# Performance work log

Measured on AMD Instinct MI355X. Metric: run time of the kernel, lower is better.

Reference implementation:

```python
import jax, jax.numpy as jnp
import numpy as np
from jax import lax

# dims: B batch, L seq len, D channels, N SSM state size
BATCH, L, D, N = 8, 2048, 256, 64
MIN_DELTA = 1e-6
EPS = 1e-6


def setup_inputs() -> dict:
    key = jax.random.key(0)
    k0, k1, k2, k3, k4 = jax.random.split(key, 5)
    x = jax.random.normal(k0, (BATCH, L, D), dtype=jnp.float32)
    # log_A chosen so A = softplus(log_A) is small -> discrete_A^L stays finite in fp32
    log_A = -jax.random.normal(k1, (N, N), dtype=jnp.float32) - 3.0
    Bp = jax.random.normal(k2, (D, N), dtype=jnp.float32) * 0.02
    Cp = jax.random.normal(k3, (D, N), dtype=jnp.float32) * 0.02
    log_delta = jnp.full((D,), -8.0, dtype=jnp.float32)  # dt ~ 3.4e-4 (stability)
    skip_D = jnp.ones((D,), dtype=jnp.float32)
    W_out = jax.random.normal(k4, (D, D), dtype=jnp.float32) * (1.0 / np.sqrt(D))
    b_out = jnp.zeros((D,), dtype=jnp.float32)
    return dict(x=x, log_A=log_A, Bp=Bp, Cp=Cp, log_delta=log_delta,
                skip_D=skip_D, W_out=W_out, b_out=b_out)


def reference(x, log_A, Bp, Cp, log_delta, skip_D, W_out, b_out):
    Bsz, Lx, Dx = x.shape
    # --- discretize ---
    A = jax.nn.softplus(log_A)                                  # [N,N]
    dt = jax.nn.softplus(log_delta) + MIN_DELTA                 # [D]
    dA = jax.vmap(jax.scipy.linalg.expm)(A[None] * dt[:, None, None])  # [D,N,N]
    I = jnp.eye(A.shape[0], dtype=A.dtype)
    X = jnp.linalg.solve(A + EPS * I, Bp.T)                     # [N,D] = A^{-1} B^T
    dB = jnp.einsum('dnm,dm->dn', dA - I, X.T)                  # [D,N]
    # --- kernel k[d,l] = C_d . (dA_d)^l dB_d, via sequential recurrence (same math
    # as the explicit A-power loop, carrying the vector instead of the matrix) ---
    def step(v, _):
        return jnp.einsum('dnm,dm->dn', dA, v), jnp.sum(Cp * v, axis=-1)
    _, ks = lax.scan(step, dB, None, length=Lx)                 # ks: [L,D]
    k = ks.T                                                    # [D,L]
    # --- grouped causal conv1d: y[b,d,t] = sum_tau k[d,tau] x[b,d,t-tau] ---
    w = jnp.flip(k, -1)[:, None, :]                             # [D,1,L]
    y = lax.conv_general_dilated(
        jnp.transpose(x, (0, 2, 1)), w, (1,), [(Lx - 1, 0)],
        dimension_numbers=('NCH', 'OIH', 'NCH'), feature_group_count=Dx)
    y = jnp.transpose(y, (0, 2, 1))                             # [B,L,D]
    return (y + x * skip_D) @ W_out.T + b_out
```

## Files before the change

kernel.cpp:

```cpp
#include <hip/hip_runtime.h>

#define Bz 8
#define Lz 2048
#define Dz 256
#define Nz 64
#define SP 68
#define SA 65
#define SAK 72
#define SKB 136
#define SE 68
#define KE 4
#define KP 7

typedef __attribute__((ext_vector_type(8))) short bf16x8;
typedef __attribute__((ext_vector_type(4))) float f32x4;

__device__ __forceinline__ float softplusf(float x) {
  return (x > 20.f) ? x : log1pf(expf(x));
}

__device__ __forceinline__ unsigned short f2bf(float f) {
  unsigned int u = __float_as_uint(f);
  u += 0x7fffu + ((u >> 16) & 1u);
  return (unsigned short)(u >> 16);
}

__device__ __forceinline__ void pmm_acc(const float* __restrict__ LA,
                                        const float* __restrict__ LB,
                                        float* acc, int n, int q) {
  float arow[64];
#pragma unroll
  for (int mm = 0; mm < 16; ++mm) {
    const float4 a4 = *(const float4*)(LA + n * SP + mm * 4);
    arow[4 * mm + 0] = a4.x; arow[4 * mm + 1] = a4.y;
    arow[4 * mm + 2] = a4.z; arow[4 * mm + 3] = a4.w;
  }
#pragma unroll
  for (int i = 0; i < 16; ++i) acc[i] = 0.f;
#pragma unroll 8
  for (int m = 0; m < 64; ++m) {
    const float4 b0 = *(const float4*)(LB + m * SP + q * 16 + 0);
    const float4 b1 = *(const float4*)(LB + m * SP + q * 16 + 4);
    const float4 b2 = *(const float4*)(LB + m * SP + q * 16 + 8);
    const float4 b3 = *(const float4*)(LB + m * SP + q * 16 + 12);
    const float a = arow[m];
    acc[0]  = fmaf(a, b0.x, acc[0]);  acc[1]  = fmaf(a, b0.y, acc[1]);
    acc[2]  = fmaf(a, b0.z, acc[2]);  acc[3]  = fmaf(a, b0.w, acc[3]);
    acc[4]  = fmaf(a, b1.x, acc[4]);  acc[5]  = fmaf(a, b1.y, acc[5]);
    acc[6]  = fmaf(a, b1.z, acc[6]);  acc[7]  = fmaf(a, b1.w, acc[7]);
    acc[8]  = fmaf(a, b2.x, acc[8]);  acc[9]  = fmaf(a, b2.y, acc[9]);
    acc[10] = fmaf(a, b2.z, acc[10]); acc[11] = fmaf(a, b2.w, acc[11]);
    acc[12] = fmaf(a, b3.x, acc[12]); acc[13] = fmaf(a, b3.y, acc[13]);
    acc[14] = fmaf(a, b3.z, acc[14]); acc[15] = fmaf(a, b3.w, acc[15]);
  }
}

__global__ __launch_bounds__(256) void s4_xt(const float* __restrict__ x,
                                             float* __restrict__ xT,
                                             const float* __restrict__ log_A,
                                             float* __restrict__ Apow) {
  if (blockIdx.x == 0 && blockIdx.y == 0) {
    const int i = blockIdx.z * 512 + threadIdx.x;
    Apow[i] = softplusf(log_A[i]);
    Apow[i + 256] = softplusf(log_A[i + 256]);
  }
  __shared__ float tile[64][69];
  const int t0 = blockIdx.x * 64, d0 = blockIdx.y * 64, b = blockIdx.z;
  const int rr = threadIdx.x >> 4;
  const int c4 = (threadIdx.x & 15) * 4;
#pragma unroll
  for (int p = 0; p < 4; ++p) {
    const int row = p * 16 + rr;
    const float4 v = *(const float4*)(x + ((size_t)b * Lz + t0 + row) * Dz + d0 + c4);
    tile[row][c4 + 0] = v.x; tile[row][c4 + 1] = v.y;
    tile[row][c4 + 2] = v.z; tile[row][c4 + 3] = v.w;
  }
  __syncthreads();
#pragma unroll
  for (int p = 0; p < 4; ++p) {
    const int dd = p * 16 + rr;
    float4 o;
    o.x = tile[c4 + 0][dd]; o.y = tile[c4 + 1][dd];
    o.z = tile[c4 + 2][dd]; o.w = tile[c4 + 3][dd];
    *(float4*)(xT + ((size_t)(d0 + dd) * Bz + b) * Lz + t0 + c4) = o;
  }
}

__global__ __launch_bounds__(256, 1) void s4_buildpow(
    float* __restrict__ Apow, const float* __restrict__ Bp,
    const float* __restrict__ Cp, const float* __restrict__ log_delta,
    float* __restrict__ Gk, float* __restrict__ Qk,
    float* __restrict__ kloc, float* __restrict__ dts) {
  __shared__ float As[Nz * SA];
  __shared__ float Pst[KP + 1][Nz];
  __shared__ float Qst[KE + 1][Nz];
  __shared__ float Pv[Nz], Qv[Nz], dBs[Nz];
  __shared__ float prA[4][Nz + 8], prB[4][Nz + 8];
  __shared__ float zp[KE + 1][17], zs[KE + 1];
  __shared__ alignas(16) float PA[Nz * SP];
  __shared__ alignas(16) float PB[Nz * SP];
  const int tid = threadIdx.x;
  const int d = blockIdx.x;
  const int n = tid & 63, qq = tid >> 6;

  if (d >= Dz) {
    const int role = d - Dz;
#pragma unroll
    for (int i = 0; i < 4; ++i) {
      const int e = (tid + 256 * i) * 4;
      const int r = e >> 6, c = e & 63;
      const float4 v = *(const float4*)(Apow + e);
      *(float4*)&PA[r * SP + c] = v;
      *(float4*)&PB[r * SP + c] = v;
    }
    __syncthreads();
    float acc[16];
    pmm_acc(PA, PB, acc, n, qq);
    if (role == 0) {
      float* O = Apow + (size_t)1 * 4096;
#pragma unroll
      for (int v = 0; v < 4; ++v) {
        float4 o;
        o.x = acc[4 * v]; o.y = acc[4 * v + 1];
        o.z = acc[4 * v + 2]; o.w = acc[4 * v + 3];
        *(float4*)(O + n * 64 + qq * 16 + 4 * v) = o;
      }
      return;
    }
    __syncthreads();
#pragma unroll
    for (int i = 0; i < 16; ++i) {
      PB[n * SP + qq * 16 + i] = acc[i];
      if (role == 2) PA[n * SP + qq * 16 + i] = acc[i];
    }
    __syncthreads();
    pmm_acc(PA, PB, acc, n, qq);
    float* O = Apow + (size_t)(role + 1) * 4096;
#pragma unroll
    for (int v = 0; v < 4; ++v) {
      float4 o;
      o.x = acc[4 * v]; o.y = acc[4 * v + 1];
      o.z = acc[4 * v + 2]; o.w = acc[4 * v + 3];
      *(float4*)(O + n * 64 + qq * 16 + 4 * v) = o;
    }
    return;
  }

  const float dt = softplusf(log_delta[d]) + 1e-6f;
#pragma unroll
  for (int i = 0; i < 4; ++i) {
    const int e = (tid + 256 * i) * 4;
    const int r = e >> 6, c = e & 63;
    const float4 v = *(const float4*)(Apow + e);
    As[r * SA + c] = v.x; As[r * SA + c + 1] = v.y;
    As[r * SA + c + 2] = v.z; As[r * SA + c + 3] = v.w;
  }
  if (tid < 64) {
    const float bv = Bp[d * Nz + tid], cv = Cp[d * Nz + tid];
    Pv[tid] = bv; Pst[0][tid] = bv;
    Qv[tid] = cv; Qst[0][tid] = cv;
  }
  __syncthreads();
#pragma unroll 1
  for (int k = 1; k <= KP; ++k) {
    float pp = 0.f, pq = 0.f;
#pragma unroll
    for (int mm = 0; mm < 16; ++mm) {
      const int m = qq * 16 + mm;
      pp += As[n * SA + m] * Pv[m];
      pq += As[m * SA + n] * Qv[m];
    }
    prA[qq][n] = pp; prB[qq][n] = pq;
    __syncthreads();
    if (tid < 64) {
      const float np = prA[0][tid] + prA[1][tid] + prA[2][tid] + prA[3][tid];
      Pv[tid] = np; Pst[k][tid] = np;
      if (k <= KE) {
        const float nq = prB[0][tid] + prB[1][tid] + prB[2][tid] + prB[3][tid];
        Qv[tid] = nq; Qst[k][tid] = nq;
      }
    }
    __syncthreads();
  }
  const float dtc0 = dt;
  const float dtc1 = dt * dt * 0.5f;
  const float dtc2 = dtc1 * dt * (1.f / 3.f);
  const float dtc3 = dtc2 * dt * 0.25f;
  if (tid < 64) {
    dBs[tid] = dtc0 * Pst[0][tid] + dtc1 * Pst[1][tid] +
               dtc2 * Pst[2][tid] + dtc3 * Pst[3][tid];
#pragma unroll
    for (int k = 0; k <= KE; ++k) {
      Gk[(size_t)d * ((KE + 1) * 64) + k * 64 + tid] =
          dtc0 * Pst[k][tid] + dtc1 * Pst[k + 1][tid] +
          dtc2 * Pst[k + 2][tid] + dtc3 * Pst[k + 3][tid];
      Qk[(size_t)d * ((KE + 1) * 64) + k * 64 + tid] = Qst[k][tid];
    }
  }
  __syncthreads();
  if (tid < (KE + 1) * 16) {
    const int k = tid >> 4, seg = tid & 15;
    float s = 0.f;
#pragma unroll
    for (int i = 0; i < 4; ++i) s += Qst[k][seg * 4 + i] * dBs[seg * 4 + i];
    zp[k][seg] = s;
  }
  __syncthreads();
  if (tid <= KE) {
    float s = 0.f;
#pragma unroll
    for (int seg = 0; seg < 16; ++seg) s += zp[tid][seg];
    zs[tid] = s;
  }
  __syncthreads();
  if (tid < 64) {
    const float rdt = (float)tid * dt;
    float c = 1.f, acc = zs[0];
#pragma unroll
    for (int k = 1; k <= KE; ++k) { c *= rdt / (float)k; acc += c * zs[k]; }
    kloc[d * 64 + tid] = acc;
  }
  if (tid == 0) dts[d] = dt;
}

__global__ __launch_bounds__(512, 2) void s4_scan7(
    const float* __restrict__ xT, const float* __restrict__ Apow,
    const float* __restrict__ Gk, const float* __restrict__ dts,
    float* __restrict__ S) {
  __shared__ alignas(16) float Es[Nz * SE];
  __shared__ alignas(16) float Us[Nz * SE];
  __shared__ float Gs[(KE + 1) * Nz];
  __shared__ float CTs[KE + 1][66];
  __shared__ alignas(16) float Sw[Bz][SE];
  __shared__ alignas(16) float Xw[Bz][SE];
  const int d = blockIdx.x;
  const int tid = threadIdx.x;
  const int w = tid >> 6;
  const int n = tid & 63;
  const float dt = dts[d];
  if (tid < 65) {
    const float rdt = (float)tid * dt;
    float c = 1.f;
    CTs[0][tid] = 1.f;
#pragma unroll
    for (int k = 1; k <= KE; ++k) { c *= rdt / (float)k; CTs[k][tid] = c; }
  }
  for (int idx = tid; idx < (KE + 1) * 64; idx += 512)
    Gs[idx] = Gk[(size_t)d * ((KE + 1) * 64) + idx];
  {
    float ea[8];
#pragma unroll
    for (int i = 0; i < 8; ++i) ea[i] = 0.f;
    const float dt64 = 64.f * dt;
    float ce = 1.f;
#pragma unroll
    for (int k = 1; k <= KE; ++k) {
      ce *= dt64 / (float)k;
      const float* Ak = Apow + (size_t)(k - 1) * 4096;
#pragma unroll
      for (int i = 0; i < 8; ++i)
        ea[i] = fmaf(ce, Ak[tid + 512 * i], ea[i]);
    }
#pragma unroll
    for (int i = 0; i < 8; ++i) {
      const int e = tid + 512 * i;
      const int r = e >> 6, c = e & 63;
      Es[r * SE + c] = ea[i] + ((r == c) ? 1.f : 0.f);
    }
  }
  __syncthreads();
  {
    const int r = tid >> 3, j0 = (tid & 7) * 8;
    float g0 = Gs[0 * 64 + r], g1 = Gs[1 * 64 + r], g2 = Gs[2 * 64 + r];
    float g3 = Gs[3 * 64 + r], g4 = Gs[4 * 64 + r];
#pragma unroll
    for (int jj = 0; jj < 8; ++jj) {
      const int j = j0 + jj;
      float u = g0 * CTs[0][63 - j];
      u = fmaf(g1, CTs[1][63 - j], u);
      u = fmaf(g2, CTs[2][63 - j], u);
      u = fmaf(g3, CTs[3][63 - j], u);
      u = fmaf(g4, CTs[4][63 - j], u);
      Us[r * SE + j] = u;
    }
  }
  __syncthreads();
  float Erow[64], Urow[64];
#pragma unroll
  for (int mb = 0; mb < 16; ++mb) {
    const float4 e4 = *(const float4*)&Es[n * SE + 4 * mb];
    Erow[4 * mb + 0] = e4.x; Erow[4 * mb + 1] = e4.y;
    Erow[4 * mb + 2] = e4.z; Erow[4 * mb + 3] = e4.w;
    const float4 u4 = *(const float4*)&Us[n * SE + 4 * mb];
    Urow[4 * mb + 0] = u4.x; Urow[4 * mb + 1] = u4.y;
    Urow[4 * mb + 2] = u4.z; Urow[4 * mb + 3] = u4.w;
  }
  const float* xw = xT + ((size_t)d * Bz + w) * (size_t)Lz;
  float* Sd = S + (size_t)d * (32 * 8 * 64) + w * 64 + n;
  float s = 0.f;
  float xcur = xw[n];
  float xnxt = xw[64 + n];
#pragma unroll 1
  for (int c = 0; c < 32; ++c) {
    Sw[w][n] = s;
    Xw[w][n] = xcur;
    Sd[(size_t)c * 512] = s;
    const int cl = (c + 2 < 32) ? (c + 2) : 31;
    const float xnew = xw[cl * 64 + n];
    float a0 = 0.f, a1 = 0.f, a2 = 0.f, a3 = 0.f;
#pragma unroll
    for (int mb = 0; mb < 16; ++mb) {
      const float4 sb = *(const float4*)&Sw[w][4 * mb];
      a0 = fmaf(Erow[4 * mb + 0], sb.x, a0);
      a1 = fmaf(Erow[4 * mb + 1], sb.y, a1);
      a2 = fmaf(Erow[4 * mb + 2], sb.z, a2);
      a3 = fmaf(Erow[4 * mb + 3], sb.w, a3);
    }
#pragma unroll
    for (int jb = 0; jb < 16; ++jb) {
      const float4 xb = *(const float4*)&Xw[w][4 * jb];
      a0 = fmaf(Urow[4 * jb + 0], xb.x, a0);
      a1 = fmaf(Urow[4 * jb + 1], xb.y, a1);
      a2 = fmaf(Urow[4 * jb + 2], xb.z, a2);
      a3 = fmaf(Urow[4 * jb + 3], xb.w, a3);
    }
    s = (a0 + a1) + (a2 + a3);
    xcur = xnxt; xnxt = xnew;
  }
}

__global__ __launch_bounds__(256, 4) void s4_out7(
    const float* __restrict__ xT, const float* __restrict__ S,
    const float* __restrict__ Qk, const float* __restrict__ kloc,
    const float* __restrict__ dts, const float* __restrict__ skip_D,
    unsigned short* __restrict__ yb) {
  __shared__ alignas(16) unsigned short Msb[64 * SKB];
  __shared__ alignas(16) unsigned short Zsb[64 * SKB];
  __shared__ float Qs[(KE + 1) * Nz];
  __shared__ float CT[KE + 1][66];
  __shared__ unsigned short kxb[64];
  const int d = blockIdx.x;
  const int ch = blockIdx.y;
  const int tid = threadIdx.x;
  const int wave = tid >> 6, lane = tid & 63;
  const int quad = lane >> 4, lq = lane & 15;
  const float dt = dts[d];
  if (tid < 65) {
    const float rdt = (float)tid * dt;
    float c = 1.f;
    CT[0][tid] = 1.f;
#pragma unroll
    for (int k = 1; k <= KE; ++k) { c *= rdt / (float)k; CT[k][tid] = c; }
  }
  for (int idx = tid; idx < (KE + 1) * 64; idx += 256)
    Qs[idx] = Qk[(size_t)d * ((KE + 1) * 64) + idx];
  if (tid < 64)
    kxb[tid] = f2bf(kloc[d * 64 + tid] + ((tid == 0) ? skip_D[d] : 0.f));

  const float* xd = xT + (size_t)d * Bz * Lz;
  const float* Sd = S + (size_t)d * (32 * 8 * 64);
#pragma unroll
  for (int p = 0; p < 8; ++p) {
    const int u = tid + 256 * p;
    const int col = u >> 5;
    const int sub = u & 31;
    const int k0 = sub * 4;
    const int bb = col & 7, ccl = col >> 3;
    const int cc = ch * 8 + ccl;
    const float* src = (k0 < 64)
        ? (Sd + cc * 512 + bb * 64 + k0)
        : (xd + (size_t)bb * Lz + cc * 64 + (k0 - 64));
    const float4 v = *(const float4*)src;
    ushort4 o;
    o.x = f2bf(v.x); o.y = f2bf(v.y); o.z = f2bf(v.z); o.w = f2bf(v.w);
    *(ushort4*)&Zsb[col * SKB + k0] = o;
  }
  __syncthreads();

#pragma unroll
  for (int i = 0; i < 16; ++i) {
    const int e = tid + 256 * i;
    const int r = e >> 6, m = e & 63;
    float w = 0.f;
#pragma unroll
    for (int k = 0; k <= KE; ++k) w = fmaf(CT[k][r + 1], Qs[k * 64 + m], w);
    Msb[r * SKB + m] = f2bf(w);
  }
#pragma unroll
  for (int i = 0; i < 16; ++i) {
    const int e = tid + 256 * i;
    const int r = e >> 6, j = e & 63;
    Msb[r * SKB + 64 + j] = (j <= r) ? kxb[r - j] : (unsigned short)0;
  }
  __syncthreads();

  f32x4 acc[4];
#pragma unroll
  for (int ni = 0; ni < 4; ++ni)
#pragma unroll
    for (int i = 0; i < 4; ++i) acc[ni][i] = 0.f;
#pragma unroll
  for (int ks = 0; ks < 4; ++ks) {
    const bf16x8 af =
        *(const bf16x8*)&Msb[(wave * 16 + lq) * SKB + ks * 32 + quad * 8];
#pragma unroll
    for (int ni = 0; ni < 4; ++ni) {
      const bf16x8 bfr =
          *(const bf16x8*)&Zsb[(ni * 16 + lq) * SKB + ks * 32 + quad * 8];
      acc[ni] = __builtin_amdgcn_mfma_f32_16x16x32_bf16(af, bfr, acc[ni], 0, 0, 0);
    }
  }
#pragma unroll
  for (int ni = 0; ni < 4; ++ni) {
    const int col = ni * 16 + lq;
    const int bb = col & 7, ccl = col >> 3;
    const int cc = ch * 8 + ccl;
    ushort4 o;
    o.x = f2bf(acc[ni][0]); o.y = f2bf(acc[ni][1]);
    o.z = f2bf(acc[ni][2]); o.w = f2bf(acc[ni][3]);
    *(ushort4*)(yb + ((size_t)d * Bz + bb) * Lz + cc * 64 + wave * 16 + quad * 4) = o;
  }
}

__global__ __launch_bounds__(256, 2) void s4_gemm5(
    const unsigned short* __restrict__ yb, const float* __restrict__ Wo,
    const float* __restrict__ bo, float* __restrict__ out) {
  __shared__ alignas(16) unsigned short LA[128 * SAK];
  __shared__ alignas(16) unsigned short LB[64 * SAK];
  const int tid = threadIdx.x;
  const int wave = tid >> 6, lane = tid & 63;
  const int quad = lane >> 4, lq = lane & 15;
  const int r0 = blockIdx.x * 128;
  const int c0 = blockIdx.y * 64;
  const int brow = r0 >> 11, t0 = r0 & 2047;
  const int ad = tid & 63;
  const int atg = tid >> 6;
  const int bc = tid >> 2;
  const int bko = tid & 3;
  f32x4 acc[2][4];
#pragma unroll
  for (int mi = 0; mi < 2; ++mi)
#pragma unroll
    for (int ni = 0; ni < 4; ++ni)
#pragma unroll
      for (int i = 0; i < 4; ++i) acc[mi][ni][i] = 0.f;
#pragma unroll 1
  for (int ks = 0; ks < 4; ++ks) {
    const int k0 = ks * 64;
    {
      const unsigned short* src =
          yb + ((size_t)(k0 + ad) * Bz + brow) * Lz + t0 + atg * 32;
#pragma unroll
      for (int h = 0; h < 4; ++h) {
        const bf16x8 v = *(const bf16x8*)(src + h * 8);
#pragma unroll
        for (int j = 0; j < 8; ++j)
          LA[(atg * 32 + h * 8 + j) * SAK + ad] = (unsigned short)v[j];
      }
    }
#pragma unroll
    for (int half = 0; half < 2; ++half) {
      const int kk = half * 32 + bko * 8;
      const float* wsrc = Wo + (size_t)(c0 + bc) * Dz + k0 + kk;
      const float4 w0 = *(const float4*)(wsrc);
      const float4 w1 = *(const float4*)(wsrc + 4);
      bf16x8 wv;
      wv[0] = (short)f2bf(w0.x); wv[1] = (short)f2bf(w0.y);
      wv[2] = (short)f2bf(w0.z); wv[3] = (short)f2bf(w0.w);
      wv[4] = (short)f2bf(w1.x); wv[5] = (short)f2bf(w1.y);
      wv[6] = (short)f2bf(w1.z); wv[7] = (short)f2bf(w1.w);
      *(bf16x8*)&LB[bc * SAK + kk] = wv;
    }
    __syncthreads();
#pragma unroll
    for (int ksub = 0; ksub < 2; ++ksub) {
      bf16x8 af[2], bfr[4];
#pragma unroll
      for (int mi = 0; mi < 2; ++mi)
        af[mi] = *(const bf16x8*)
            &LA[(wave * 32 + mi * 16 + lq) * SAK + ksub * 32 + quad * 8];
#pragma unroll
      for (int ni = 0; ni < 4; ++ni)
        bfr[ni] = *(const bf16x8*)
            &LB[(ni * 16 + lq) * SAK + ksub * 32 + quad * 8];
#pragma unroll
      for (int mi = 0; mi < 2; ++mi)
#pragma unroll
        for (int ni = 0; ni < 4; ++ni)
          acc[mi][ni] = __builtin_amdgcn_mfma_f32_16x16x32_bf16(
              af[mi], bfr[ni], acc[mi][ni], 0, 0, 0);
    }
    __syncthreads();
  }
  float bb[4];
#pragma unroll
  for (int ni = 0; ni < 4; ++ni) bb[ni] = bo[c0 + ni * 16 + lq];
#pragma unroll
  for (int mi = 0; mi < 2; ++mi)
#pragma unroll
    for (int i = 0; i < 4; ++i) {
      const int row = r0 + wave * 32 + mi * 16 + quad * 4 + i;
#pragma unroll
      for (int ni = 0; ni < 4; ++ni)
        out[(size_t)row * Dz + c0 + ni * 16 + lq] = acc[mi][ni][i] + bb[ni];
    }
}

extern "C" void kernel_launch(void* const* d_in, const int* in_sizes, int n_in,
                              void* d_out, int out_size, void* d_ws, size_t ws_size,
                              hipStream_t stream) {
  const float* x         = (const float*)d_in[0];
  const float* log_A     = (const float*)d_in[1];
  const float* Bp        = (const float*)d_in[2];
  const float* Cp        = (const float*)d_in[3];
  const float* log_delta = (const float*)d_in[4];
  const float* skip_D    = (const float*)d_in[5];
  const float* W_out     = (const float*)d_in[6];
  const float* b_out     = (const float*)d_in[7];
  float* out = (float*)d_out;

  float* xT   = (float*)d_ws;
  float* ybf  = xT + (size_t)Dz * Bz * Lz;
  float* S    = ybf + (size_t)Dz * Bz * Lz;
  float* Apow = S + (size_t)Dz * (32 * 8 * 64);
  float* Gk   = Apow + (size_t)8 * 4096;
  float* Qk   = Gk + (size_t)Dz * (KE + 1) * 64;
  float* kloc = Qk + (size_t)Dz * (KE + 1) * 64;
  float* dts  = kloc + (size_t)Dz * 64;
  unsigned short* yb = (unsigned short*)ybf;

  hipLaunchKernelGGL(s4_xt, dim3(Lz / 64, Dz / 64, Bz), dim3(256), 0, stream,
                     x, xT, log_A, Apow);
  hipLaunchKernelGGL(s4_buildpow, dim3(Dz + 3), dim3(256), 0, stream,
                     Apow, Bp, Cp, log_delta, Gk, Qk, kloc, dts);
  hipLaunchKernelGGL(s4_scan7, dim3(Dz), dim3(512), 0, stream,
                     xT, Apow, Gk, dts, S);
  hipLaunchKernelGGL(s4_out7, dim3(Dz, 4), dim3(256), 0, stream,
                     xT, S, Qk, kloc, dts, skip_D, yb);
  hipLaunchKernelGGL(s4_gemm5, dim3((Bz * Lz) / 128, Dz / 64), dim3(256), 0, stream,
                     yb, W_out, b_out, out);
}
```

Measured before the change: 137.8 us.

## Fuse chunk-state scan and output MFMA kernels into one per-channel kernel

Merges the chunked state scan and the output convolution kernel into a single block per channel. Chunk states stay in LDS instead of round-tripping through global memory, and LDS is overlaid between the scan's E/U matrices and the bf16 Z tiles. The cost is a much larger LDS footprint, occupancy cut to one block per CU, and only 256 blocks doing the output MFMA work, previously spread over 1024 blocks.

```diff
diff --git a/kernel.cpp b/kernel.cpp
--- a/kernel.cpp
+++ b/kernel.cpp
@@ -223,16 +223,23 @@
   if (tid == 0) dts[d] = dt;
 }
 
-__global__ __launch_bounds__(512, 2) void s4_scan7(
+__global__ __launch_bounds__(512, 1) void s4_scanout(
     const float* __restrict__ xT, const float* __restrict__ Apow,
-    const float* __restrict__ Gk, const float* __restrict__ dts,
-    float* __restrict__ S) {
-  __shared__ alignas(16) float Es[Nz * SE];
-  __shared__ alignas(16) float Us[Nz * SE];
-  __shared__ float Gs[(KE + 1) * Nz];
+    const float* __restrict__ Gk, const float* __restrict__ Qk,
+    const float* __restrict__ kloc, const float* __restrict__ dts,
+    const float* __restrict__ skip_D, unsigned short* __restrict__ yb) {
+  __shared__ alignas(16) float SB[32][Bz][64];
+  __shared__ alignas(16) char ovl[Nz * SE * 4 * 2];
+  __shared__ float Gq[(KE + 1) * Nz];
   __shared__ float CTs[KE + 1][66];
   __shared__ alignas(16) float Sw[Bz][SE];
   __shared__ alignas(16) float Xw[Bz][SE];
+  __shared__ alignas(16) unsigned short Msb[64 * SKB];
+  __shared__ unsigned short kxb[64];
+  float* Es = (float*)ovl;
+  float* Us = (float*)(ovl + Nz * SE * 4);
+  unsigned short* Zsb = (unsigned short*)ovl;
+
   const int d = blockIdx.x;
   const int tid = threadIdx.x;
   const int w = tid >> 6;
@@ -246,7 +253,7 @@
     for (int k = 1; k <= KE; ++k) { c *= rdt / (float)k; CTs[k][tid] = c; }
   }
   for (int idx = tid; idx < (KE + 1) * 64; idx += 512)
-    Gs[idx] = Gk[(size_t)d * ((KE + 1) * 64) + idx];
+    Gq[idx] = Gk[(size_t)d * ((KE + 1) * 64) + idx];
   {
     float ea[8];
 #pragma unroll
@@ -271,8 +278,8 @@
   __syncthreads();
   {
     const int r = tid >> 3, j0 = (tid & 7) * 8;
-    float g0 = Gs[0 * 64 + r], g1 = Gs[1 * 64 + r], g2 = Gs[2 * 64 + r];
-    float g3 = Gs[3 * 64 + r], g4 = Gs[4 * 64 + r];
+    float g0 = Gq[0 * 64 + r], g1 = Gq[1 * 64 + r], g2 = Gq[2 * 64 + r];
+    float g3 = Gq[3 * 64 + r], g4 = Gq[4 * 64 + r];
 #pragma unroll
     for (int jj = 0; jj < 8; ++jj) {
       const int j = j0 + jj;
@@ -296,7 +303,6 @@
     Urow[4 * mb + 2] = u4.z; Urow[4 * mb + 3] = u4.w;
   }
   const float* xw = xT + ((size_t)d * Bz + w) * (size_t)Lz;
-  float* Sd = S + (size_t)d * (32 * 8 * 64) + w * 64 + n;
   float s = 0.f;
   float xcur = xw[n];
   float xnxt = xw[64 + n];
@@ -304,7 +310,7 @@
   for (int c = 0; c < 32; ++c) {
     Sw[w][n] = s;
     Xw[w][n] = xcur;
-    Sd[(size_t)c * 512] = s;
+    SB[c][w][n] = s;
     const int cl = (c + 2 < 32) ? (c + 2) : 31;
     const float xnew = xw[cl * 64 + n];
     float a0 = 0.f, a1 = 0.f, a2 = 0.f, a3 = 0.f;
@@ -327,98 +333,99 @@
     s = (a0 + a1) + (a2 + a3);
     xcur = xnxt; xnxt = xnew;
   }
-}
-
-__global__ __launch_bounds__(256, 4) void s4_out7(
-    const float* __restrict__ xT, const float* __restrict__ S,
-    const float* __restrict__ Qk, const float* __restrict__ kloc,
-    const float* __restrict__ dts, const float* __restrict__ skip_D,
-    unsigned short* __restrict__ yb) {
-  __shared__ alignas(16) unsigned short Msb[64 * SKB];
-  __shared__ alignas(16) unsigned short Zsb[64 * SKB];
-  __shared__ float Qs[(KE + 1) * Nz];
-  __shared__ float CT[KE + 1][66];
-  __shared__ unsigned short kxb[64];
-  const int d = blockIdx.x;
-  const int ch = blockIdx.y;
-  const int tid = threadIdx.x;
+  __syncthreads();
+
+  for (int idx = tid; idx < (KE + 1) * 64; idx += 512)
+    Gq[idx] = Qk[(size_t)d * ((KE + 1) * 64) + idx];
+  if (tid < 64)
+    kxb[tid] = f2bf(kloc[d * 64 + tid] + ((tid == 0) ? skip_D[d] : 0.f));
+
   const int wave = tid >> 6, lane = tid & 63;
   const int quad = lane >> 4, lq = lane & 15;
-  const float dt = dts[d];
-  if (tid < 65) {
-    const float rdt = (float)tid * dt;
-    float c = 1.f;
-    CT[0][tid] = 1.f;
-#pragma unroll
-    for (int k = 1; k <= KE; ++k) { c *= rdt / (float)k; CT[k][tid] = c; }
-  }
-  for (int idx = tid; idx < (KE + 1) * 64; idx += 256)
-    Qs[idx] = Qk[(size_t)d * ((KE + 1) * 64) + idx];
-  if (tid < 64)
-    kxb[tid] = f2bf(kloc[d * 64 + tid] + ((tid == 0) ? skip_D[d] : 0.f));
-
+  const int g = wave >> 2, wv = wave & 3;
   const float* xd = xT + (size_t)d * Bz * Lz;
-  const float* Sd = S + (size_t)d * (32 * 8 * 64);
-#pragma unroll
-  for (int p = 0; p < 8; ++p) {
-    const int u = tid + 256 * p;
-    const int col = u >> 5;
-    const int sub = u & 31;
+
+#pragma unroll
+  for (int i = 0; i < 8; ++i) {
+    const int u = tid + 512 * i;
+    const int zi = u >> 11, rem = u & 2047;
+    const int col = rem >> 5, sub = rem & 31;
     const int k0 = sub * 4;
     const int bb = col & 7, ccl = col >> 3;
-    const int cc = ch * 8 + ccl;
-    const float* src = (k0 < 64)
-        ? (Sd + cc * 512 + bb * 64 + k0)
-        : (xd + (size_t)bb * Lz + cc * 64 + (k0 - 64));
-    const float4 v = *(const float4*)src;
+    const int cc = zi * 8 + ccl;
+    float4 v;
+    if (k0 < 64) v = *(const float4*)&SB[cc][bb][k0];
+    else v = *(const float4*)(xd + (size_t)bb * Lz + cc * 64 + (k0 - 64));
     ushort4 o;
     o.x = f2bf(v.x); o.y = f2bf(v.y); o.z = f2bf(v.z); o.w = f2bf(v.w);
-    *(ushort4*)&Zsb[col * SKB + k0] = o;
-  }
-  __syncthreads();
-
-#pragma unroll
-  for (int i = 0; i < 16; ++i) {
-    const int e = tid + 256 * i;
+    *(ushort4*)&Zsb[(size_t)zi * 64 * SKB + col * SKB + k0] = o;
+  }
+  __syncthreads();
+
+#pragma unroll
+  for (int i = 0; i < 8; ++i) {
+    const int e = tid + 512 * i;
     const int r = e >> 6, m = e & 63;
-    float w = 0.f;
-#pragma unroll
-    for (int k = 0; k <= KE; ++k) w = fmaf(CT[k][r + 1], Qs[k * 64 + m], w);
-    Msb[r * SKB + m] = f2bf(w);
-  }
-#pragma unroll
-  for (int i = 0; i < 16; ++i) {
-    const int e = tid + 256 * i;
+    float wv2 = 0.f;
+#pragma unroll
+    for (int k = 0; k <= KE; ++k) wv2 = fmaf(CTs[k][r + 1], Gq[k * 64 + m], wv2);
+    Msb[r * SKB + m] = f2bf(wv2);
+  }
+#pragma unroll
+  for (int i = 0; i < 8; ++i) {
+    const int e = tid + 512 * i;
     const int r = e >> 6, j = e & 63;
     Msb[r * SKB + 64 + j] = (j <= r) ? kxb[r - j] : (unsigned short)0;
   }
   __syncthreads();
 
-  f32x4 acc[4];
-#pragma unroll
-  for (int ni = 0; ni < 4; ++ni)
-#pragma unroll
-    for (int i = 0; i < 4; ++i) acc[ni][i] = 0.f;
-#pragma unroll
-  for (int ks = 0; ks < 4; ++ks) {
-    const bf16x8 af =
-        *(const bf16x8*)&Msb[(wave * 16 + lq) * SKB + ks * 32 + quad * 8];
+#pragma unroll 1
+  for (int p = 0; p < 2; ++p) {
+    f32x4 acc[4];
+#pragma unroll
+    for (int ni = 0; ni < 4; ++ni)
+#pragma unroll
+      for (int i = 0; i < 4; ++i) acc[ni][i] = 0.f;
+#pragma unroll
+    for (int ks = 0; ks < 4; ++ks) {
+      const bf16x8 af =
+          *(const bf16x8*)&Msb[(wv * 16 + lq) * SKB + ks * 32 + quad * 8];
+#pragma unroll
+      for (int ni = 0; ni < 4; ++ni) {
+        const bf16x8 bfr = *(const bf16x8*)
+            &Zsb[(size_t)g * 64 * SKB + (ni * 16 + lq) * SKB + ks * 32 + quad * 8];
+        acc[ni] = __builtin_amdgcn_mfma_f32_16x16x32_bf16(af, bfr, acc[ni], 0, 0, 0);
+      }
+    }
 #pragma unroll
     for (int ni = 0; ni < 4; ++ni) {
-      const bf16x8 bfr =
-          *(const bf16x8*)&Zsb[(ni * 16 + lq) * SKB + ks * 32 + quad * 8];
-      acc[ni] = __builtin_amdgcn_mfma_f32_16x16x32_bf16(af, bfr, acc[ni], 0, 0, 0);
-    }
-  }
-#pragma unroll
-  for (int ni = 0; ni < 4; ++ni) {
-    const int col = ni * 16 + lq;
-    const int bb = col & 7, ccl = col >> 3;
-    const int cc = ch * 8 + ccl;
-    ushort4 o;
-    o.x = f2bf(acc[ni][0]); o.y = f2bf(acc[ni][1]);
-    o.z = f2bf(acc[ni][2]); o.w = f2bf(acc[ni][3]);
-    *(ushort4*)(yb + ((size_t)d * Bz + bb) * Lz + cc * 64 + wave * 16 + quad * 4) = o;
+      const int col = ni * 16 + lq;
+      const int bb = col & 7, ccl = col >> 3;
+      const int cc = (2 * p + g) * 8 + ccl;
+      ushort4 o;
+      o.x = f2bf(acc[ni][0]); o.y = f2bf(acc[ni][1]);
+      o.z = f2bf(acc[ni][2]); o.w = f2bf(acc[ni][3]);
+      *(ushort4*)(yb + ((size_t)d * Bz + bb) * Lz + cc * 64 + wv * 16 + quad * 4) = o;
+    }
+    if (p == 0) {
+      __syncthreads();
+#pragma unroll
+      for (int i = 0; i < 8; ++i) {
+        const int u = tid + 512 * i;
+        const int zi = u >> 11, rem = u & 2047;
+        const int col = rem >> 5, sub = rem & 31;
+        const int k0 = sub * 4;
+        const int bb = col & 7, ccl = col >> 3;
+        const int cc = (2 + zi) * 8 + ccl;
+        float4 v;
+        if (k0 < 64) v = *(const float4*)&SB[cc][bb][k0];
+        else v = *(const float4*)(xd + (size_t)bb * Lz + cc * 64 + (k0 - 64));
+        ushort4 o;
+        o.x = f2bf(v.x); o.y = f2bf(v.y); o.z = f2bf(v.z); o.w = f2bf(v.w);
+        *(ushort4*)&Zsb[(size_t)zi * 64 * SKB + col * SKB + k0] = o;
+      }
+      __syncthreads();
+    }
   }
 }
 
@@ -533,10 +540,8 @@
                      x, xT, log_A, Apow);
   hipLaunchKernelGGL(s4_buildpow, dim3(Dz + 3), dim3(256), 0, stream,
                      Apow, Bp, Cp, log_delta, Gk, Qk, kloc, dts);
-  hipLaunchKernelGGL(s4_scan7, dim3(Dz), dim3(512), 0, stream,
-                     xT, Apow, Gk, dts, S);
-  hipLaunchKernelGGL(s4_out7, dim3(Dz, 4), dim3(256), 0, stream,
-                     xT, S, Qk, kloc, dts, skip_D, yb);
+  hipLaunchKernelGGL(s4_scanout, dim3(Dz), dim3(512), 0, stream,
+                     xT, Apow, Gk, Qk, kloc, dts, skip_D, yb);
   hipLaunchKernelGGL(s4_gemm5, dim3((Bz * Lz) / 128, Dz / 64), dim3(256), 0, stream,
                      yb, W_out, b_out, out);
 }
```

Result: slower. 140.9 us (+2.2%).
